# Kernel tuning notes

Measured on AMD Instinct MI355X. Metric: run time of the kernel, lower is better.

## Reference

```python
import jax, jax.numpy as jnp
import numpy as np

B, F, S, D = 256, 8, 200, 64
H = 36  # hidden units per field
EPS = 1e-3  # Dice BN epsilon


def setup_inputs() -> dict:
    key0 = jax.random.key(0)
    ks = jax.random.split(key0, 8)
    query = jax.random.normal(ks[0], (B, F, D), dtype=jnp.float32)
    key = jax.random.normal(ks[1], (B, F, S, D), dtype=jnp.float32)
    sequence_num = jax.random.randint(ks[2], (B, F), 1, S + 1, dtype=jnp.int32)
    W_h = jax.random.normal(ks[3], (F, 3 * D, H), dtype=jnp.float32) * 0.05
    b_h = jnp.zeros((F, H), dtype=jnp.float32)
    alpha = jnp.zeros((F,), dtype=jnp.float32)
    W_o = jax.random.normal(ks[4], (F, H, 1), dtype=jnp.float32) * 0.05
    b_o = jnp.zeros((F, 1), dtype=jnp.float32)
    return {"query": query, "key": key, "W_h": W_h, "b_h": b_h,
            "alpha": alpha, "W_o": W_o, "b_o": b_o,
            "sequence_num": sequence_num, "training": 1}


def reference(query, key, W_h, b_h, alpha, W_o, b_o, sequence_num, training):
    # query: [B,F,D], key: [B,F,S,D]
    q = query[:, :, None, :]                      # broadcast instead of tile
    qb = jnp.broadcast_to(q, key.shape)           # [B,F,S,D]
    cat = jnp.concatenate([key, qb, q - key], axis=-1)  # [B,F,S,3D]
    # per-field Dense(36), vectorized across fields
    h = jnp.einsum('bfsc,fch->bfsh', cat, W_h) + b_h[None, :, None, :]
    # Dice: BatchNorm (no affine, training-mode batch stats over batch+seq per field/feature)
    mean = h.mean(axis=(0, 2), keepdims=True)
    var = h.var(axis=(0, 2), keepdims=True)
    p = jax.nn.sigmoid((h - mean) * jax.lax.rsqrt(var + EPS))
    h = (alpha[None, :, None, None] * (1.0 - p) + p) * h
    # per-field Dense(1) -> attention scores [B,F,S]
    scores = jnp.einsum('bfsh,fh->bfs', h, W_o[:, :, 0]) + b_o[None, :, 0, None]
    # mask invalid positions and softmax over sequence
    mask = jnp.arange(key.shape[2])[None, None, :] < sequence_num[:, :, None]
    scores = jnp.where(mask, scores, -jnp.inf)
    attn = jax.nn.softmax(scores, axis=-1)        # [B,F,S]
    # weighted sum over sequence -> [B,F,D]
    return jnp.einsum('bfs,bfsd->bfd', attn, key)
```

## Files before the change

kernel.cpp:

```cpp
#include <hip/hip_runtime.h>
#include <math.h>

#define NB 256
#define NF 8
#define NS 200
#define ND 64
#define NH 36
#define MT 13
#define EPSV 1e-3f
#define NCPY 8

#define WS_SUM 0
#define WS_SQ  (NCPY * 288)
#define WS_QT  (2 * NCPY * 288)
#define WS_WK  (WS_QT + 2048 * 48)
#define WS_KC  (WS_WK + (NF * 48 * ND) / 2)

typedef __attribute__((ext_vector_type(8))) short short8;
typedef __attribute__((ext_vector_type(4))) float f32x4;

__device__ __forceinline__ unsigned short f32_to_bf16(float x) {
    unsigned u = __float_as_uint(x);
    unsigned r = u + 0x7FFFu + ((u >> 16) & 1u);
    return (unsigned short)(r >> 16);
}
__device__ __forceinline__ float bf16_to_f32(unsigned short h) {
    return __uint_as_float(((unsigned)h) << 16);
}
__device__ __forceinline__ short8 cvt8(float4 a, float4 b) {
    short8 r;
    r[0] = (short)f32_to_bf16(a.x); r[1] = (short)f32_to_bf16(a.y);
    r[2] = (short)f32_to_bf16(a.z); r[3] = (short)f32_to_bf16(a.w);
    r[4] = (short)f32_to_bf16(b.x); r[5] = (short)f32_to_bf16(b.y);
    r[6] = (short)f32_to_bf16(b.z); r[7] = (short)f32_to_bf16(b.w);
    return r;
}

__global__ __launch_bounds__(256) void k_prep(
    const float* __restrict__ query, const float* __restrict__ W_h,
    const float* __restrict__ b_h, float* __restrict__ ws)
{
    const int blk = blockIdx.x, tid = threadIdx.x;
    if (blk < NF) {
        const int f = blk;
        const float* Wf = W_h + (size_t)f * (3 * ND * NH);
        unsigned short* wk = (unsigned short*)(ws + WS_WK) + f * (48 * ND);
        for (int i = tid; i < 48 * ND; i += 256) {
            int h = i >> 6, d = i & 63;
            float v = (h < NH) ? (Wf[d * NH + h] - Wf[(2 * ND + d) * NH + h]) : 0.f;
            wk[h * ND + d] = f32_to_bf16(v);
        }
    } else if (blk == NF) {
        for (int i = tid; i < 2 * NCPY * 288; i += 256) ws[i] = 0.f;
    } else {
        const int b = blk - NF - 1;
        __shared__ float qs[NF * ND];
        for (int i = tid; i < NF * ND; i += 256)
            qs[i] = query[(size_t)b * NF * ND + i];
        __syncthreads();
        for (int i = tid; i < NF * 48; i += 256) {
            int f = i / 48, h = i - f * 48;
            float acc = 0.f;
            if (h < NH) {
                const float* Wf = W_h + (size_t)f * (3 * ND * NH);
                acc = b_h[f * NH + h];
                for (int d = 0; d < ND; ++d)
                    acc += qs[f * ND + d] * (Wf[(ND + d) * NH + h] + Wf[(2 * ND + d) * NH + h]);
            }
            ws[WS_QT + (size_t)(b * NF + f) * 48 + h] = acc;
        }
    }
}

__global__ __launch_bounds__(256, 3) void k_stats(
    const float* __restrict__ key, float* __restrict__ ws)
{
    const int blk = blockIdx.x;
    const int f = blk & (NF - 1);
    const int tid = threadIdx.x;
    const int lane = tid & 63;
    const int wv = tid >> 6;
    const int col = lane & 15;
    const int quad = lane >> 4;

    __shared__ float sumP[48], sqP[48];
    if (tid < 48) { sumP[tid] = 0.f; sqP[tid] = 0.f; }
    __syncthreads();

    const float* kbase = key + (size_t)blk * (NS * ND);
    const unsigned short* wk = (const unsigned short*)(ws + WS_WK) + f * (48 * ND);
    unsigned short* kc = (unsigned short*)(ws + WS_KC);

    float4 pf[4][4];
    #pragma unroll
    for (int t = 0; t < 4; ++t) {
        const int mt = wv + 4 * t;
        if (mt < MT) {
            const int s = 16 * mt + col;
            const float4* p = (const float4*)(kbase + (size_t)(s < NS ? s : NS - 1) * ND + quad * 8);
            pf[t][0] = p[0]; pf[t][1] = p[1];
            pf[t][2] = p[8]; pf[t][3] = p[9];
        }
    }

    short8 bfr[3][2];
    float qv[3];
    #pragma unroll
    for (int nt = 0; nt < 3; ++nt) {
        #pragma unroll
        for (int ks = 0; ks < 2; ++ks)
            bfr[nt][ks] = *(const short8*)&wk[(nt * 16 + col) * ND + ks * 32 + quad * 8];
        qv[nt] = ws[WS_QT + (size_t)blk * 48 + nt * 16 + col];
    }

    float s_sum[3] = {0.f, 0.f, 0.f}, s_sq[3] = {0.f, 0.f, 0.f};
    #pragma unroll
    for (int t = 0; t < 4; ++t) {
        const int mt = wv + 4 * t;
        if (mt < MT) {
            short8 ah0 = cvt8(pf[t][0], pf[t][1]);
            short8 ah1 = cvt8(pf[t][2], pf[t][3]);
            const size_t cb = ((size_t)(blk * MT + mt) * 64 + lane) * 16;
            *(short8*)&kc[cb] = ah0;
            *(short8*)&kc[cb + 8] = ah1;
            #pragma unroll
            for (int nt = 0; nt < 3; ++nt) {
                f32x4 acc = {qv[nt], qv[nt], qv[nt], qv[nt]};
                acc = __builtin_amdgcn_mfma_f32_16x16x32_bf16(ah0, bfr[nt][0], acc, 0, 0, 0);
                acc = __builtin_amdgcn_mfma_f32_16x16x32_bf16(ah1, bfr[nt][1], acc, 0, 0, 0);
                #pragma unroll
                for (int r = 0; r < 4; ++r) {
                    int srow = 16 * mt + quad * 4 + r;
                    if (srow < NS) { float v = acc[r]; s_sum[nt] += v; s_sq[nt] += v * v; }
                }
            }
        }
    }
    #pragma unroll
    for (int nt = 0; nt < 3; ++nt) {
        float sv = s_sum[nt], qq = s_sq[nt];
        sv += __shfl_xor(sv, 16, 64); sv += __shfl_xor(sv, 32, 64);
        qq += __shfl_xor(qq, 16, 64); qq += __shfl_xor(qq, 32, 64);
        if (quad == 0) {
            atomicAdd(&sumP[nt * 16 + col], sv);
            atomicAdd(&sqP[nt * 16 + col], qq);
        }
    }
    __syncthreads();
    if (tid < NH) {
        const int c = (blk >> 3) & (NCPY - 1);
        atomicAdd(&ws[WS_SUM + c * 288 + f * NH + tid], sumP[tid]);
        atomicAdd(&ws[WS_SQ  + c * 288 + f * NH + tid], sqP[tid]);
    }
}

__global__ __launch_bounds__(256, 4) void k_attn(
    const float* __restrict__ alpha,
    const float* __restrict__ W_o, const float* __restrict__ b_o,
    const int* __restrict__ seqn, const float* __restrict__ ws,
    float* __restrict__ out)
{
    const int blk = blockIdx.x;
    const int f = blk & (NF - 1);
    const int tid = threadIdx.x;
    const int lane = tid & 63;
    const int wv = tid >> 6;
    const int col = lane & 15;
    const int quad = lane >> 4;

    __shared__ float sw[208];
    __shared__ float redM[4], redS[4];
    __shared__ float pout[4][64];
    __shared__ float ssum[NH], ssq[NH];

    const unsigned short* wk = (const unsigned short*)(ws + WS_WK) + f * (48 * ND);
    const unsigned short* kc = (const unsigned short*)(ws + WS_KC);
    const float inv_n = 1.f / (float)(NB * NS);

    if (tid < NH) {
        float a = 0.f, b2 = 0.f;
        #pragma unroll
        for (int c = 0; c < NCPY; ++c) {
            a  += ws[WS_SUM + c * 288 + f * NH + tid];
            b2 += ws[WS_SQ  + c * 288 + f * NH + tid];
        }
        ssum[tid] = a; ssq[tid] = b2;
    }

    short8 kah[4][2];
    kah[3][0] = short8{0,0,0,0,0,0,0,0};
    kah[3][1] = short8{0,0,0,0,0,0,0,0};
    #pragma unroll
    for (int t = 0; t < 4; ++t) {
        const int mt = wv + 4 * t;
        if (mt < MT) {
            const size_t cb = ((size_t)(blk * MT + mt) * 64 + lane) * 16;
            kah[t][0] = *(const short8*)&kc[cb];
            kah[t][1] = *(const short8*)&kc[cb + 8];
        }
    }
    __syncthreads();

    short8 bfr[3][2];
    float qv[3], mn[3], iv[3], wo[3];
    #pragma unroll
    for (int nt = 0; nt < 3; ++nt) {
        #pragma unroll
        for (int ks = 0; ks < 2; ++ks)
            bfr[nt][ks] = *(const short8*)&wk[(nt * 16 + col) * ND + ks * 32 + quad * 8];
        const int hh = nt * 16 + col;
        const bool hv = hh < NH;
        const int hc = hv ? hh : 0;
        qv[nt] = ws[WS_QT + (size_t)blk * 48 + hh];
        const float sm = ssum[hc];
        const float sq = ssq[hc];
        const float m = sm * inv_n;
        mn[nt] = m;
        iv[nt] = rsqrtf(fmaxf(sq * inv_n - m * m, 0.f) + EPSV);
        wo[nt] = hv ? W_o[f * NH + hh] : 0.f;
    }
    const float alf = alpha[f];
    const float bo = b_o[f];
    const int sq_n = seqn[blk];

    #pragma unroll
    for (int t = 0; t < 4; ++t) {
        const int mt = wv + 4 * t;
        if (mt < MT) {
            float part[4] = {0.f, 0.f, 0.f, 0.f};
            #pragma unroll
            for (int nt = 0; nt < 3; ++nt) {
                f32x4 acc = {qv[nt], qv[nt], qv[nt], qv[nt]};
                acc = __builtin_amdgcn_mfma_f32_16x16x32_bf16(kah[t][0], bfr[nt][0], acc, 0, 0, 0);
                acc = __builtin_amdgcn_mfma_f32_16x16x32_bf16(kah[t][1], bfr[nt][1], acc, 0, 0, 0);
                #pragma unroll
                for (int r = 0; r < 4; ++r) {
                    const float h = acc[r];
                    const float pg = 1.f / (1.f + __expf(-(h - mn[nt]) * iv[nt]));
                    part[r] += (alf + (1.f - alf) * pg) * h * wo[nt];
                }
            }
            #pragma unroll
            for (int r = 0; r < 4; ++r) {
                float v = part[r];
                v += __shfl_xor(v, 1, 64);
                v += __shfl_xor(v, 2, 64);
                v += __shfl_xor(v, 4, 64);
                v += __shfl_xor(v, 8, 64);
                const int srow = 16 * mt + quad * 4 + r;
                if (col == 0 && srow < NS) sw[srow] = v + bo;
            }
        }
    }
    __syncthreads();

    const bool valid = (tid < 208) && (tid < sq_n);
    const float sc = valid ? sw[tid] : -1e30f;
    float m = sc;
    m = fmaxf(m, __shfl_xor(m, 1, 64));  m = fmaxf(m, __shfl_xor(m, 2, 64));
    m = fmaxf(m, __shfl_xor(m, 4, 64));  m = fmaxf(m, __shfl_xor(m, 8, 64));
    m = fmaxf(m, __shfl_xor(m, 16, 64)); m = fmaxf(m, __shfl_xor(m, 32, 64));
    if (lane == 0) redM[wv] = m;
    __syncthreads();
    const float maxv = fmaxf(fmaxf(redM[0], redM[1]), fmaxf(redM[2], redM[3]));
    const float e = valid ? __expf(sc - maxv) : 0.f;
    float l = e;
    l += __shfl_xor(l, 1, 64);  l += __shfl_xor(l, 2, 64);
    l += __shfl_xor(l, 4, 64);  l += __shfl_xor(l, 8, 64);
    l += __shfl_xor(l, 16, 64); l += __shfl_xor(l, 32, 64);
    if (lane == 0) redS[wv] = l;
    __syncthreads();
    const float isum = 1.f / (redS[0] + redS[1] + redS[2] + redS[3]);
    if (tid < 208) sw[tid] = e * isum;
    __syncthreads();

    float po0[8] = {0,0,0,0,0,0,0,0}, po1[8] = {0,0,0,0,0,0,0,0};
    #pragma unroll
    for (int t = 0; t < 4; ++t) {
        const int mt = wv + 4 * t;
        if (mt < MT) {
            const float w = sw[16 * mt + col];
            #pragma unroll
            for (int j = 0; j < 8; ++j) {
                po0[j] += w * bf16_to_f32((unsigned short)kah[t][0][j]);
                po1[j] += w * bf16_to_f32((unsigned short)kah[t][1][j]);
            }
        }
    }
    #pragma unroll
    for (int off = 1; off <= 8; off <<= 1) {
        #pragma unroll
        for (int j = 0; j < 8; ++j) {
            po0[j] += __shfl_xor(po0[j], off, 64);
            po1[j] += __shfl_xor(po1[j], off, 64);
        }
    }
    if (col == 0) {
        #pragma unroll
        for (int j = 0; j < 8; ++j) {
            pout[wv][quad * 8 + j] = po0[j];
            pout[wv][32 + quad * 8 + j] = po1[j];
        }
    }
    __syncthreads();
    if (tid < 64)
        out[(size_t)blk * ND + tid] =
            pout[0][tid] + pout[1][tid] + pout[2][tid] + pout[3][tid];
}

extern "C" void kernel_launch(void* const* d_in, const int* in_sizes, int n_in,
                              void* d_out, int out_size, void* d_ws, size_t ws_size,
                              hipStream_t stream) {
    const float* query = (const float*)d_in[0];
    const float* key   = (const float*)d_in[1];
    const float* W_h   = (const float*)d_in[2];
    const float* b_h   = (const float*)d_in[3];
    const float* alpha = (const float*)d_in[4];
    const float* W_o   = (const float*)d_in[5];
    const float* b_o   = (const float*)d_in[6];
    const int*   seqn  = (const int*)d_in[7];
    float* out = (float*)d_out;
    float* ws  = (float*)d_ws;

    k_prep<<<NB + NF + 1, 256, 0, stream>>>(query, W_h, b_h, ws);
    k_stats<<<NB * NF, 256, 0, stream>>>(key, ws);
    k_attn<<<NB * NF, 256, 0, stream>>>(alpha, W_o, b_o, seqn, ws, out);
}
```

Before: 212.8 us.

## Fuse prep into stats kernel and replace atomic stats with per-batch partials

Removes the separate k_prep launch. Each stats block now builds its field's bf16 weight difference in shared memory and computes its own query projection there. Global atomic accumulation of BN sums is replaced by per-(f,b) partial writes, which k_attn reduces over 256 batches. This saves a launch and the atomic contention and removes the need to zero the accumulators. In exchange, every block redundantly recomputes the weight conversion from W_h, and each attention block reads 256x72 partials.

New measurement: 229.5 us. +7.8%, slower.

```diff
diff --git a/kernel.cpp b/kernel.cpp
--- a/kernel.cpp
+++ b/kernel.cpp
@@ -8,13 +8,11 @@
 #define NH 36
 #define MT 13
 #define EPSV 1e-3f
-#define NCPY 8
-
-#define WS_SUM 0
-#define WS_SQ  (NCPY * 288)
-#define WS_QT  (2 * NCPY * 288)
-#define WS_WK  (WS_QT + 2048 * 48)
-#define WS_KC  (WS_WK + (NF * 48 * ND) / 2)
+
+#define WS_QT   0
+#define WS_WKS  (2048 * 48)
+#define WS_PART (WS_WKS + 12288)
+#define WS_KC   (WS_PART + NF * NB * 72)
 
 typedef __attribute__((ext_vector_type(8))) short short8;
 typedef __attribute__((ext_vector_type(4))) float f32x4;
@@ -36,62 +34,32 @@
     return r;
 }
 
-__global__ __launch_bounds__(256) void k_prep(
-    const float* __restrict__ query, const float* __restrict__ W_h,
-    const float* __restrict__ b_h, float* __restrict__ ws)
-{
-    const int blk = blockIdx.x, tid = threadIdx.x;
-    if (blk < NF) {
-        const int f = blk;
-        const float* Wf = W_h + (size_t)f * (3 * ND * NH);
-        unsigned short* wk = (unsigned short*)(ws + WS_WK) + f * (48 * ND);
-        for (int i = tid; i < 48 * ND; i += 256) {
-            int h = i >> 6, d = i & 63;
-            float v = (h < NH) ? (Wf[d * NH + h] - Wf[(2 * ND + d) * NH + h]) : 0.f;
-            wk[h * ND + d] = f32_to_bf16(v);
-        }
-    } else if (blk == NF) {
-        for (int i = tid; i < 2 * NCPY * 288; i += 256) ws[i] = 0.f;
-    } else {
-        const int b = blk - NF - 1;
-        __shared__ float qs[NF * ND];
-        for (int i = tid; i < NF * ND; i += 256)
-            qs[i] = query[(size_t)b * NF * ND + i];
-        __syncthreads();
-        for (int i = tid; i < NF * 48; i += 256) {
-            int f = i / 48, h = i - f * 48;
-            float acc = 0.f;
-            if (h < NH) {
-                const float* Wf = W_h + (size_t)f * (3 * ND * NH);
-                acc = b_h[f * NH + h];
-                for (int d = 0; d < ND; ++d)
-                    acc += qs[f * ND + d] * (Wf[(ND + d) * NH + h] + Wf[(2 * ND + d) * NH + h]);
-            }
-            ws[WS_QT + (size_t)(b * NF + f) * 48 + h] = acc;
-        }
-    }
-}
-
 __global__ __launch_bounds__(256, 3) void k_stats(
-    const float* __restrict__ key, float* __restrict__ ws)
+    const float* __restrict__ query, const float* __restrict__ key,
+    const float* __restrict__ W_h, const float* __restrict__ b_h,
+    float* __restrict__ ws)
 {
     const int blk = blockIdx.x;
     const int f = blk & (NF - 1);
+    const int b = blk >> 3;
     const int tid = threadIdx.x;
     const int lane = tid & 63;
     const int wv = tid >> 6;
     const int col = lane & 15;
     const int quad = lane >> 4;
 
+    __shared__ float qs[ND];
+    __shared__ __align__(16) unsigned short wkL[48 * ND];
+    __shared__ float qt_sh[48];
     __shared__ float sumP[48], sqP[48];
-    if (tid < 48) { sumP[tid] = 0.f; sqP[tid] = 0.f; }
-    __syncthreads();
 
     const float* kbase = key + (size_t)blk * (NS * ND);
-    const unsigned short* wk = (const unsigned short*)(ws + WS_WK) + f * (48 * ND);
-    unsigned short* kc = (unsigned short*)(ws + WS_KC);
 
     float4 pf[4][4];
+    {
+        const float4 z4 = {0.f, 0.f, 0.f, 0.f};
+        pf[3][0] = z4; pf[3][1] = z4; pf[3][2] = z4; pf[3][3] = z4;
+    }
     #pragma unroll
     for (int t = 0; t < 4; ++t) {
         const int mt = wv + 4 * t;
@@ -103,16 +71,48 @@
         }
     }
 
+    const float* Wf = W_h + (size_t)f * (3 * ND * NH);
+    if (tid < ND) qs[tid] = query[(size_t)blk * ND + tid];
+    if (tid < 48) {
+        sumP[tid] = 0.f; sqP[tid] = 0.f;
+        qt_sh[tid] = (tid < NH) ? b_h[f * NH + tid] : 0.f;
+    }
+    for (int i = tid; i < 48 * ND; i += 256) {
+        int h = i >> 6, d = i & 63;
+        float v = (h < NH) ? (Wf[d * NH + h] - Wf[(2 * ND + d) * NH + h]) : 0.f;
+        wkL[i] = f32_to_bf16(v);
+    }
+    __syncthreads();
+
+    if (tid < 240) {
+        const int h = tid % 48, seg = tid / 48;
+        if (h < NH) {
+            int d0 = seg * 13, d1 = d0 + 13; if (d1 > ND) d1 = ND;
+            float acc = 0.f;
+            for (int d = d0; d < d1; ++d)
+                acc += qs[d] * (Wf[(ND + d) * NH + h] + Wf[(2 * ND + d) * NH + h]);
+            atomicAdd(&qt_sh[h], acc);
+        }
+    }
+    __syncthreads();
+
+    if (tid < 48) ws[WS_QT + (size_t)blk * 48 + tid] = qt_sh[tid];
+    if (b == 0) {
+        unsigned short* wkg = (unsigned short*)(ws + WS_WKS) + f * (48 * ND);
+        for (int i = tid; i < 48 * ND; i += 256) wkg[i] = wkL[i];
+    }
+
     short8 bfr[3][2];
     float qv[3];
     #pragma unroll
     for (int nt = 0; nt < 3; ++nt) {
         #pragma unroll
         for (int ks = 0; ks < 2; ++ks)
-            bfr[nt][ks] = *(const short8*)&wk[(nt * 16 + col) * ND + ks * 32 + quad * 8];
-        qv[nt] = ws[WS_QT + (size_t)blk * 48 + nt * 16 + col];
-    }
-
+            bfr[nt][ks] = *(const short8*)&wkL[(nt * 16 + col) * ND + ks * 32 + quad * 8];
+        qv[nt] = qt_sh[nt * 16 + col];
+    }
+
+    unsigned short* kc = (unsigned short*)(ws + WS_KC);
     float s_sum[3] = {0.f, 0.f, 0.f}, s_sq[3] = {0.f, 0.f, 0.f};
     #pragma unroll
     for (int t = 0; t < 4; ++t) {
@@ -148,9 +148,9 @@
     }
     __syncthreads();
     if (tid < NH) {
-        const int c = (blk >> 3) & (NCPY - 1);
-        atomicAdd(&ws[WS_SUM + c * 288 + f * NH + tid], sumP[tid]);
-        atomicAdd(&ws[WS_SQ  + c * 288 + f * NH + tid], sqP[tid]);
+        float* P = ws + WS_PART + ((size_t)f * NB + b) * 72;
+        P[tid] = sumP[tid];
+        P[36 + tid] = sqP[tid];
     }
 }
 
@@ -171,20 +171,21 @@
     __shared__ float sw[208];
     __shared__ float redM[4], redS[4];
     __shared__ float pout[4][64];
+    __shared__ float red2[2][72];
     __shared__ float ssum[NH], ssq[NH];
 
-    const unsigned short* wk = (const unsigned short*)(ws + WS_WK) + f * (48 * ND);
+    const unsigned short* wk = (const unsigned short*)(ws + WS_WKS) + f * (48 * ND);
     const unsigned short* kc = (const unsigned short*)(ws + WS_KC);
     const float inv_n = 1.f / (float)(NB * NS);
 
-    if (tid < NH) {
-        float a = 0.f, b2 = 0.f;
-        #pragma unroll
-        for (int c = 0; c < NCPY; ++c) {
-            a  += ws[WS_SUM + c * 288 + f * NH + tid];
-            b2 += ws[WS_SQ  + c * 288 + f * NH + tid];
-        }
-        ssum[tid] = a; ssq[tid] = b2;
+    if (tid < 144) {
+        const int j = tid % 72, half = tid / 72;
+        const float* P = ws + WS_PART + (size_t)f * NB * 72;
+        float a = 0.f;
+        #pragma unroll 8
+        for (int bb = half * 128; bb < half * 128 + 128; ++bb)
+            a += P[(size_t)bb * 72 + j];
+        red2[half][j] = a;
     }
 
     short8 kah[4][2];
@@ -198,6 +199,11 @@
             kah[t][0] = *(const short8*)&kc[cb];
             kah[t][1] = *(const short8*)&kc[cb + 8];
         }
+    }
+    __syncthreads();
+    if (tid < NH) {
+        ssum[tid] = red2[0][tid] + red2[1][tid];
+        ssq[tid]  = red2[0][36 + tid] + red2[1][36 + tid];
     }
     __syncthreads();
 
@@ -322,7 +328,6 @@
     float* out = (float*)d_out;
     float* ws  = (float*)d_ws;
 
-    k_prep<<<NB + NF + 1, 256, 0, stream>>>(query, W_h, b_h, ws);
-    k_stats<<<NB * NF, 256, 0, stream>>>(key, ws);
+    k_stats<<<NB * NF, 256, 0, stream>>>(query, key, W_h, b_h, ws);
     k_attn<<<NB * NF, 256, 0, stream>>>(alpha, W_o, b_o, seqn, ws, out);
 }
```
